# Performance work log

Hardware: AMD Instinct MI355X
Metric: run time of the kernel (lower is better)

Reference implementation:

```python
import jax, jax.numpy as jnp
import numpy as np

N_NODES = 200000
IN_DIM = 128
HID = 64
WALK_LEN = 16          # max_step + 1
NUM_WALKS = 16         # = hidden_graphs, walks per graph
N_GRAPHS = 1024
PEN = 32
N_CLASSES = 10
BN_EPS = 1e-5


def setup_inputs() -> dict:
    key = jax.random.key(0)
    ks = jax.random.split(key, 16)
    x = jax.random.normal(ks[0], (N_NODES, IN_DIM), dtype=jnp.float32)
    walks = jax.random.randint(ks[1], (N_GRAPHS * NUM_WALKS, WALK_LEN), 0, N_NODES)
    # each graph contributes NUM_WALKS consecutive walks
    walk_batch = jnp.repeat(jnp.arange(N_GRAPHS), NUM_WALKS)
    s = 1.0 / np.sqrt(HID)
    return {
        "x": x,
        "walks": walks,
        "walk_batch": walk_batch,
        "W_enc": jax.random.normal(ks[2], (HID, IN_DIM), jnp.float32) / np.sqrt(IN_DIM),
        "b_enc": jnp.zeros((HID,), jnp.float32),
        "W_ih": jax.random.uniform(ks[3], (3 * HID, HID), jnp.float32, -s, s),
        "W_hh": jax.random.uniform(ks[4], (3 * HID, HID), jnp.float32, -s, s),
        "b_ih": jax.random.uniform(ks[5], (3 * HID,), jnp.float32, -s, s),
        "b_hh": jax.random.uniform(ks[6], (3 * HID,), jnp.float32, -s, s),
        "gamma": jnp.ones((HID,), jnp.float32),
        "beta": jnp.zeros((HID,), jnp.float32),
        "W1": jax.random.normal(ks[7], (PEN, HID), jnp.float32) / np.sqrt(HID),
        "b1": jnp.zeros((PEN,), jnp.float32),
        "W2": jax.random.normal(ks[8], (N_CLASSES, PEN), jnp.float32) / np.sqrt(PEN),
        "b2": jnp.zeros((N_CLASSES,), jnp.float32),
    }


def _gru_cell(h, xt, W_ih, W_hh, b_ih, b_hh):
    # PyTorch GRU gate math
    gi = xt @ W_ih.T + b_ih            # [W, 3H]
    gh = h @ W_hh.T + b_hh             # [W, 3H]
    i_r, i_z, i_n = jnp.split(gi, 3, axis=-1)
    h_r, h_z, h_n = jnp.split(gh, 3, axis=-1)
    r = jax.nn.sigmoid(i_r + h_r)
    z = jax.nn.sigmoid(i_z + h_z)
    n = jnp.tanh(i_n + r * h_n)
    return (1.0 - z) * n + z * h


def reference(x, walks, walk_batch, W_enc, b_enc, W_ih, W_hh, b_ih, b_hh,
              gamma, beta, W1, b1, W2, b2):
    # feature encoder on all nodes, then gather along walks
    x_enc = x @ W_enc.T + b_enc                     # [N, H]
    walk_feats = x_enc[walks]                       # [W, L, H] gather
    xs = jnp.swapaxes(walk_feats, 0, 1)             # [L, W, H]

    def step(h, xt):
        return _gru_cell(h, xt, W_ih, W_hh, b_ih, b_hh), None

    h0 = jnp.zeros((walks.shape[0], HID), walk_feats.dtype)
    h_final, _ = jax.lax.scan(step, h0, xs)         # [W, H] last hidden state

    # segment-mean pooling per graph
    seg_sum = jax.ops.segment_sum(h_final, walk_batch, num_segments=N_GRAPHS)
    cnt = jax.ops.segment_sum(jnp.ones((walks.shape[0],), h_final.dtype),
                              walk_batch, num_segments=N_GRAPHS)
    graph_enc = seg_sum / jnp.maximum(cnt, 1.0)[:, None]   # [B, H]

    # BatchNorm1d (training mode: batch statistics, biased variance)
    mean = jnp.mean(graph_enc, axis=0)
    var = jnp.mean(jnp.square(graph_enc - mean), axis=0)
    gn = (graph_enc - mean) / jnp.sqrt(var + BN_EPS) * gamma + beta

    h1 = jax.nn.relu(gn @ W1.T + b1)                # dropout p=0 -> identity
    logits = h1 @ W2.T + b2
    return jax.nn.log_softmax(logits, axis=1)
```

## Files before the change

kernel.cpp:

```cpp
#include <hip/hip_runtime.h>
#include <stdint.h>

typedef _Float16 half8 __attribute__((ext_vector_type(8)));
typedef _Float16 half4 __attribute__((ext_vector_type(4)));
typedef float f32x4 __attribute__((ext_vector_type(4)));

#define MFMA_F16(A, B, C) __builtin_amdgcn_mfma_f32_16x16x32_f16(A, B, C, 0, 0, 0)

#define NN 200000
#define NT 3125
#define GSTRIDE 512

__device__ __forceinline__ half8 cvt8(const float* p) {
  half8 a;
#pragma unroll
  for (int e = 0; e < 8; ++e) a[e] = (_Float16)p[e];
  return a;
}

__global__ __launch_bounds__(256, 2) void k_enc(const float* __restrict__ x,
                                                const float* __restrict__ Wenc,
                                                const float* __restrict__ benc,
                                                _Float16* __restrict__ xenc) {
  __shared__ float xl[64 * 128];
  __shared__ _Float16 wlds[16 * 64 * 8];

  const int tid = threadIdx.x;
  const int lane = tid & 63, wv = tid >> 6;
  const int r = lane & 15, g = lane >> 4;
  const int lrh = lane >> 5;
  const int cg = lane & 31;

  const int t0 = blockIdx.x;

  f32x4 xin[8];
#pragma unroll
  for (int i = 0; i < 8; ++i) {
    int grow = t0 * 64 + wv * 16 + 2 * i + lrh;
    if (grow >= NN) grow = NN - 1;
    xin[i] = *(const f32x4*)((const char*)(x + (size_t)grow * 128) + cg * 16);
  }

  for (int i4 = tid; i4 < 2048; i4 += 256) {
    int idx = i4 * 4;
    f32x4 v = *(const f32x4*)(Wenc + idx);
    int j = idx >> 7, k = idx & 127;
    int tile = (j >> 4) * 4 + (k >> 5);
    int ln = ((k >> 3) & 3) * 16 + (j & 15);
    half4 h;
    h[0] = (_Float16)v[0]; h[1] = (_Float16)v[1];
    h[2] = (_Float16)v[2]; h[3] = (_Float16)v[3];
    *(half4*)&wlds[(tile * 64 + ln) * 8 + (k & 7)] = h;
  }

#pragma unroll
  for (int i = 0; i < 8; ++i) {
    int row = wv * 16 + 2 * i + lrh;
    *(f32x4*)((char*)xl + row * 512 + ((cg * 16) ^ ((row & 7) << 4))) = xin[i];
  }
  __syncthreads();

  half8 W[4][4];
#pragma unroll
  for (int jt = 0; jt < 4; ++jt)
#pragma unroll
    for (int kt = 0; kt < 4; ++kt)
      W[jt][kt] = *(const half8*)&wlds[((jt * 4 + kt) * 64 + lane) * 8];

  float bb[4][4];
#pragma unroll
  for (int jt = 0; jt < 4; ++jt)
#pragma unroll
    for (int rr = 0; rr < 4; ++rr) bb[jt][rr] = benc[jt * 16 + g * 4 + rr];

  const int sw = (r & 7) << 4;

  for (int t = t0; t < NT; t += GSTRIDE) {
    int tn = t + GSTRIDE;
    if (tn < NT) {
#pragma unroll
      for (int i = 0; i < 8; ++i) {
        int grow = tn * 64 + wv * 16 + 2 * i + lrh;
        if (grow >= NN) grow = NN - 1;
        xin[i] = *(const f32x4*)((const char*)(x + (size_t)grow * 128) + cg * 16);
      }
    }

    const char* rp = (const char*)xl + (wv * 16 + r) * 512;
    f32x4 acc[4];
#pragma unroll
    for (int jt = 0; jt < 4; ++jt)
      acc[jt] = (f32x4){bb[jt][0], bb[jt][1], bb[jt][2], bb[jt][3]};

#pragma unroll
    for (int kt = 0; kt < 4; ++kt) {
      f32x4 v0 = *(const f32x4*)(rp + ((kt * 128 + g * 32) ^ sw));
      f32x4 v1 = *(const f32x4*)(rp + ((kt * 128 + g * 32 + 16) ^ sw));
      half8 a;
#pragma unroll
      for (int e = 0; e < 4; ++e) {
        a[e] = (_Float16)v0[e];
        a[4 + e] = (_Float16)v1[e];
      }
#pragma unroll
      for (int jt = 0; jt < 4; ++jt)
        acc[jt] = MFMA_F16(W[jt][kt], a, acc[jt]);
    }

    int node = t * 64 + wv * 16 + r;
    if (node < NN) {
#pragma unroll
      for (int jt = 0; jt < 4; ++jt) {
        half4 o;
        o[0] = (_Float16)acc[jt][0]; o[1] = (_Float16)acc[jt][1];
        o[2] = (_Float16)acc[jt][2]; o[3] = (_Float16)acc[jt][3];
        *(half4*)&xenc[(size_t)node * 64 + jt * 16 + g * 4] = o;
      }
    }

    if (tn < NT) {
#pragma unroll
      for (int i = 0; i < 8; ++i) {
        int row = wv * 16 + 2 * i + lrh;
        *(f32x4*)((char*)xl + row * 512 + ((cg * 16) ^ ((row & 7) << 4))) = xin[i];
      }
    }
  }
}

__global__ __launch_bounds__(256, 4) void k_gru(const _Float16* __restrict__ xenc,
                                                const int* __restrict__ walks,
                                                const float* __restrict__ Wih,
                                                const float* __restrict__ Whh,
                                                const float* __restrict__ bih,
                                                const float* __restrict__ bhh,
                                                float* __restrict__ genc) {
  __shared__ _Float16 h_lds[2][16 * 64];
  __shared__ int ids[256];

  const int tid = threadIdx.x;
  const int lane = tid & 63, wv = tid >> 6;
  const int r = lane & 15, g = lane >> 4;
  const int p = wv;
  const int gph = blockIdx.x;

  half8 Bi[3][2], Bh[3][2];
#pragma unroll
  for (int G = 0; G < 3; ++G)
#pragma unroll
    for (int kt = 0; kt < 2; ++kt) {
      int T = G * 4 + p;
      Bi[G][kt] = cvt8(Wih + (T * 16 + r) * 64 + kt * 32 + g * 8);
      Bh[G][kt] = cvt8(Whh + (T * 16 + r) * 64 + kt * 32 + g * 8);
    }

  if (wv == 0) {
    const int* wp = walks + gph * 256;
    int4 v = *(const int4*)(wp + lane * 4);
    int vals[4] = {v.x, v.y, v.z, v.w};
#pragma unroll
    for (int i = 0; i < 4; ++i) {
      int m = lane * 4 + i;
      ids[(m & 15) * 16 + (m >> 4)] = vals[i];
    }
  }
  for (int i = tid; i < 2048; i += 256) ((_Float16*)h_lds)[i] = (_Float16)0.f;

  __syncthreads();

  const int j0 = p * 16 + r;
  const float br_ = bih[j0] + bhh[j0];
  const float bz_ = bih[64 + j0] + bhh[64 + j0];
  const float bin_ = bih[128 + j0];
  const float bhn_ = bhh[128 + j0];

  f32x4 h = (f32x4){0.f, 0.f, 0.f, 0.f};
  const int swz = (r & 7) << 4;

  half8 AxA0, AxA1, AxB0, AxB1;
  {
    int n0 = ids[0 * 16 + r];
    const _Float16* p0 = xenc + (size_t)n0 * 64 + g * 8;
    AxA0 = *(const half8*)p0;
    AxA1 = *(const half8*)(p0 + 32);
    int n1 = ids[1 * 16 + r];
    const _Float16* p1 = xenc + (size_t)n1 * 64 + g * 8;
    AxB0 = *(const half8*)p1;
    AxB1 = *(const half8*)(p1 + 32);
  }

#define GRU_STEP(T_, RB, AX0, AX1)                                             \
  {                                                                            \
    int nid = ids[(((T_) + 2) & 15) * 16 + r];                                 \
    const _Float16* xp = xenc + (size_t)nid * 64 + g * 8;                      \
    half8 NX0 = *(const half8*)xp;                                             \
    half8 NX1 = *(const half8*)(xp + 32);                                      \
    char* rbase = (char*)&h_lds[RB][0];                                        \
    char* wbase = (char*)&h_lds[RB ^ 1][0];                                    \
    half8 Ah0 = *(const half8*)(rbase + ((r * 128 + g * 16) ^ swz));           \
    half8 Ah1 = *(const half8*)(rbase + ((r * 128 + 64 + g * 16) ^ swz));      \
    f32x4 aR = (f32x4){br_, br_, br_, br_};                                    \
    f32x4 aZ = (f32x4){bz_, bz_, bz_, bz_};                                    \
    f32x4 aN = (f32x4){bin_, bin_, bin_, bin_};                                \
    f32x4 aH = (f32x4){bhn_, bhn_, bhn_, bhn_};                                \
    aR = MFMA_F16(AX0, Bi[0][0], aR);                                          \
    aR = MFMA_F16(AX1, Bi[0][1], aR);                                          \
    aZ = MFMA_F16(AX0, Bi[1][0], aZ);                                          \
    aZ = MFMA_F16(AX1, Bi[1][1], aZ);                                          \
    aN = MFMA_F16(AX0, Bi[2][0], aN);                                          \
    aN = MFMA_F16(AX1, Bi[2][1], aN);                                          \
    aR = MFMA_F16(Ah0, Bh[0][0], aR);                                          \
    aR = MFMA_F16(Ah1, Bh[0][1], aR);                                          \
    aZ = MFMA_F16(Ah0, Bh[1][0], aZ);                                          \
    aZ = MFMA_F16(Ah1, Bh[1][1], aZ);                                          \
    aH = MFMA_F16(Ah0, Bh[2][0], aH);                                          \
    aH = MFMA_F16(Ah1, Bh[2][1], aH);                                          \
    _Pragma("unroll") for (int rr = 0; rr < 4; ++rr) {                         \
      float rg = __builtin_amdgcn_rcpf(1.f + __expf(-aR[rr]));                 \
      float zg = __builtin_amdgcn_rcpf(1.f + __expf(-aZ[rr]));                 \
      float pn = aN[rr] + rg * aH[rr];                                         \
      float e2 = __expf(2.f * pn);                                             \
      float nn = 1.f - 2.f * __builtin_amdgcn_rcpf(e2 + 1.f);                  \
      h[rr] = (1.f - zg) * nn + zg * h[rr];                                    \
    }                                                                          \
    if ((T_) < 15) {                                                           \
      _Pragma("unroll") for (int rr = 0; rr < 4; ++rr) {                       \
        int row = g * 4 + rr;                                                  \
        int byte = (row * 128 + j0 * 2) ^ ((row & 7) << 4);                    \
        *(_Float16*)(wbase + byte) = (_Float16)h[rr];                          \
      }                                                                        \
    }                                                                          \
    asm volatile("s_waitcnt lgkmcnt(0)" ::: "memory");                         \
    __builtin_amdgcn_s_barrier();                                              \
    __builtin_amdgcn_sched_barrier(0);                                         \
    AX0 = NX0;                                                                 \
    AX1 = NX1;                                                                 \
  }

  for (int t = 0; t < 16; t += 2) {
    GRU_STEP(t, 0, AxA0, AxA1);
    GRU_STEP(t + 1, 1, AxB0, AxB1);
  }
#undef GRU_STEP

  {
    float s = h[0] + h[1] + h[2] + h[3];
    s += __shfl_xor(s, 16);
    s += __shfl_xor(s, 32);
    if (g == 0) genc[gph * 64 + j0] = s * 0.0625f;
  }
}

__global__ __launch_bounds__(256) void k_post(const float* __restrict__ genc,
                                              const float* __restrict__ gamma,
                                              const float* __restrict__ beta,
                                              const float* __restrict__ W1,
                                              const float* __restrict__ b1,
                                              const float* __restrict__ W2,
                                              const float* __restrict__ b2,
                                              float* __restrict__ out) {
  __shared__ float sum_s[4][64], sq_s[4][64], sc[64], sh[64];
  __shared__ float w1[32 * 64], w2[10 * 32], bb1[32], bb2[10];
  const int tid = threadIdx.x;
  const int j = tid & 63, grp = tid >> 6;

  float s = 0.f, q = 0.f;
  for (int rr = 0; rr < 256; ++rr) {
    float v = genc[(grp * 256 + rr) * 64 + j];
    s += v;
    q += v * v;
  }
  sum_s[grp][j] = s;
  sq_s[grp][j] = q;

  for (int i = tid; i < 32 * 64; i += 256) w1[i] = W1[i];
  for (int i = tid; i < 10 * 32; i += 256) w2[i] = W2[i];
  if (tid < 32) bb1[tid] = b1[tid];
  if (tid >= 32 && tid < 42) bb2[tid - 32] = b2[tid - 32];
  __syncthreads();

  if (grp == 0) {
    float S = sum_s[0][j] + sum_s[1][j] + sum_s[2][j] + sum_s[3][j];
    float Q = sq_s[0][j] + sq_s[1][j] + sq_s[2][j] + sq_s[3][j];
    float mean = S * (1.f / 1024.f);
    float var = Q * (1.f / 1024.f) - mean * mean;
    float rstd = rsqrtf(var + 1e-5f);
    float scv = gamma[j] * rstd;
    sc[j] = scv;
    sh[j] = beta[j] - mean * scv;
  }
  __syncthreads();

  const int row = blockIdx.x * 256 + tid;
  float gn[64];
  const f32x4* gp = (const f32x4*)(genc + row * 64);
#pragma unroll
  for (int jq = 0; jq < 16; ++jq) {
    f32x4 v = gp[jq];
#pragma unroll
    for (int e = 0; e < 4; ++e) gn[jq * 4 + e] = v[e] * sc[jq * 4 + e] + sh[jq * 4 + e];
  }

  float h1[32];
#pragma unroll
  for (int i = 0; i < 32; ++i) {
    float a = bb1[i];
#pragma unroll
    for (int jj = 0; jj < 64; ++jj) a += w1[i * 64 + jj] * gn[jj];
    h1[i] = fmaxf(a, 0.f);
  }

  float lg[10];
  float mx = -1e30f;
#pragma unroll
  for (int c = 0; c < 10; ++c) {
    float a = bb2[c];
#pragma unroll
    for (int i = 0; i < 32; ++i) a += w2[c * 32 + i] * h1[i];
    lg[c] = a;
    mx = fmaxf(mx, a);
  }
  float se = 0.f;
#pragma unroll
  for (int c = 0; c < 10; ++c) se += __expf(lg[c] - mx);
  float lse = mx + __logf(se);
#pragma unroll
  for (int c = 0; c < 10; ++c) out[row * 10 + c] = lg[c] - lse;
}

extern "C" void kernel_launch(void* const* d_in, const int* in_sizes, int n_in,
                              void* d_out, int out_size, void* d_ws, size_t ws_size,
                              hipStream_t stream) {
  const float* x = (const float*)d_in[0];
  const int* walks = (const int*)d_in[1];
  const float* Wenc = (const float*)d_in[3];
  const float* benc = (const float*)d_in[4];
  const float* Wih = (const float*)d_in[5];
  const float* Whh = (const float*)d_in[6];
  const float* bih = (const float*)d_in[7];
  const float* bhh = (const float*)d_in[8];
  const float* gamma = (const float*)d_in[9];
  const float* beta = (const float*)d_in[10];
  const float* W1 = (const float*)d_in[11];
  const float* b1 = (const float*)d_in[12];
  const float* W2 = (const float*)d_in[13];
  const float* b2 = (const float*)d_in[14];
  float* out = (float*)d_out;

  char* ws = (char*)d_ws;
  _Float16* xenc = (_Float16*)ws;
  float* genc = (float*)(ws + 25600000);

  k_enc<<<dim3(GSTRIDE), dim3(256), 0, stream>>>(x, Wenc, benc, xenc);
  k_gru<<<dim3(1024), dim3(256), 0, stream>>>(xenc, walks, Wih, Whh, bih, bhh, genc);
  k_post<<<dim3(4), dim3(256), 0, stream>>>(genc, gamma, beta, W1, b1, W2, b2, out);
}
```

Before: 88.20 us.

## Process two graphs per GRU block with LDS-staged fp16 weights; widen encoder grid

The GRU kernel now runs two graphs per 512-thread block. Each block converts the GRU input and hidden weight matrices to fp16 once into shared memory in MFMA fragment order, and each wave loads its B fragments from there. Before, every wave fetched and converted fp32 weights from global memory itself. The encoder grid stride and occupancy hint also rise from 512 to 768 blocks and from 2 to 3 blocks per SM. In exchange, the GRU block uses much more LDS (about 54 KB), and the per-block weight conversion loop now sits before the barrier.

```diff
diff --git a/kernel.cpp b/kernel.cpp
--- a/kernel.cpp
+++ b/kernel.cpp
@@ -9,16 +9,9 @@
 
 #define NN 200000
 #define NT 3125
-#define GSTRIDE 512
-
-__device__ __forceinline__ half8 cvt8(const float* p) {
-  half8 a;
-#pragma unroll
-  for (int e = 0; e < 8; ++e) a[e] = (_Float16)p[e];
-  return a;
-}
-
-__global__ __launch_bounds__(256, 2) void k_enc(const float* __restrict__ x,
+#define GSTRIDE 768
+
+__global__ __launch_bounds__(256, 3) void k_enc(const float* __restrict__ x,
                                                 const float* __restrict__ Wenc,
                                                 const float* __restrict__ benc,
                                                 _Float16* __restrict__ xenc) {
@@ -128,45 +121,58 @@
   }
 }
 
-__global__ __launch_bounds__(256, 4) void k_gru(const _Float16* __restrict__ xenc,
+__global__ __launch_bounds__(512, 4) void k_gru(const _Float16* __restrict__ xenc,
                                                 const int* __restrict__ walks,
                                                 const float* __restrict__ Wih,
                                                 const float* __restrict__ Whh,
                                                 const float* __restrict__ bih,
                                                 const float* __restrict__ bhh,
                                                 float* __restrict__ genc) {
-  __shared__ _Float16 h_lds[2][16 * 64];
-  __shared__ int ids[256];
+  __shared__ _Float16 wih_lds[24 * 64 * 8];
+  __shared__ _Float16 whh_lds[24 * 64 * 8];
+  __shared__ _Float16 h_lds[2][2][16 * 64];
+  __shared__ int ids[2][256];
 
   const int tid = threadIdx.x;
   const int lane = tid & 63, wv = tid >> 6;
   const int r = lane & 15, g = lane >> 4;
-  const int p = wv;
-  const int gph = blockIdx.x;
-
-  half8 Bi[3][2], Bh[3][2];
-#pragma unroll
-  for (int G = 0; G < 3; ++G)
-#pragma unroll
-    for (int kt = 0; kt < 2; ++kt) {
-      int T = G * 4 + p;
-      Bi[G][kt] = cvt8(Wih + (T * 16 + r) * 64 + kt * 32 + g * 8);
-      Bh[G][kt] = cvt8(Whh + (T * 16 + r) * 64 + kt * 32 + g * 8);
-    }
-
-  if (wv == 0) {
+  const int p = wv & 3;
+  const int gl = wv >> 2;
+  const int gph = blockIdx.x * 2 + gl;
+
+  for (int idx = tid; idx < 192 * 64; idx += 512) {
+    int j = idx >> 6, k = idx & 63;
+    int tile = (j >> 4) * 2 + (k >> 5);
+    int ln = ((k >> 3) & 3) * 16 + (j & 15);
+    int off = (tile * 64 + ln) * 8 + (k & 7);
+    wih_lds[off] = (_Float16)Wih[idx];
+    whh_lds[off] = (_Float16)Whh[idx];
+  }
+
+  if ((wv & 3) == 0) {
     const int* wp = walks + gph * 256;
     int4 v = *(const int4*)(wp + lane * 4);
     int vals[4] = {v.x, v.y, v.z, v.w};
 #pragma unroll
     for (int i = 0; i < 4; ++i) {
       int m = lane * 4 + i;
-      ids[(m & 15) * 16 + (m >> 4)] = vals[i];
-    }
-  }
-  for (int i = tid; i < 2048; i += 256) ((_Float16*)h_lds)[i] = (_Float16)0.f;
+      ids[gl][(m & 15) * 16 + (m >> 4)] = vals[i];
+    }
+  }
+
+  for (int i = tid; i < 4096; i += 512) ((_Float16*)h_lds)[i] = (_Float16)0.f;
 
   __syncthreads();
+
+  half8 Bi[3][2], Bh[3][2];
+#pragma unroll
+  for (int G = 0; G < 3; ++G)
+#pragma unroll
+    for (int kt = 0; kt < 2; ++kt) {
+      int T = G * 4 + p;
+      Bi[G][kt] = *(const half8*)&wih_lds[((T * 2 + kt) * 64 + lane) * 8];
+      Bh[G][kt] = *(const half8*)&whh_lds[((T * 2 + kt) * 64 + lane) * 8];
+    }
 
   const int j0 = p * 16 + r;
   const float br_ = bih[j0] + bhh[j0];
@@ -179,11 +185,11 @@
 
   half8 AxA0, AxA1, AxB0, AxB1;
   {
-    int n0 = ids[0 * 16 + r];
+    int n0 = ids[gl][0 * 16 + r];
     const _Float16* p0 = xenc + (size_t)n0 * 64 + g * 8;
     AxA0 = *(const half8*)p0;
     AxA1 = *(const half8*)(p0 + 32);
-    int n1 = ids[1 * 16 + r];
+    int n1 = ids[gl][1 * 16 + r];
     const _Float16* p1 = xenc + (size_t)n1 * 64 + g * 8;
     AxB0 = *(const half8*)p1;
     AxB1 = *(const half8*)(p1 + 32);
@@ -191,12 +197,12 @@
 
 #define GRU_STEP(T_, RB, AX0, AX1)                                             \
   {                                                                            \
-    int nid = ids[(((T_) + 2) & 15) * 16 + r];                                 \
+    int nid = ids[gl][(((T_) + 2) & 15) * 16 + r];                             \
     const _Float16* xp = xenc + (size_t)nid * 64 + g * 8;                      \
     half8 NX0 = *(const half8*)xp;                                             \
     half8 NX1 = *(const half8*)(xp + 32);                                      \
-    char* rbase = (char*)&h_lds[RB][0];                                        \
-    char* wbase = (char*)&h_lds[RB ^ 1][0];                                    \
+    char* rbase = (char*)&h_lds[gl][RB][0];                                    \
+    char* wbase = (char*)&h_lds[gl][RB ^ 1][0];                                \
     half8 Ah0 = *(const half8*)(rbase + ((r * 128 + g * 16) ^ swz));           \
     half8 Ah1 = *(const half8*)(rbase + ((r * 128 + 64 + g * 16) ^ swz));      \
     f32x4 aR = (f32x4){br_, br_, br_, br_};                                    \
@@ -352,6 +358,6 @@
   float* genc = (float*)(ws + 25600000);
 
   k_enc<<<dim3(GSTRIDE), dim3(256), 0, stream>>>(x, Wenc, benc, xenc);
-  k_gru<<<dim3(1024), dim3(256), 0, stream>>>(xenc, walks, Wih, Whh, bih, bhh, genc);
+  k_gru<<<dim3(512), dim3(512), 0, stream>>>(xenc, walks, Wih, Whh, bih, bhh, genc);
   k_post<<<dim3(4), dim3(256), 0, stream>>>(genc, gamma, beta, W1, b1, W2, b2, out);
 }
```

Result: faster. 82.04 us (-7.0%).
